# Kernel optimization log

Measured on AMD Instinct MI355X. Metric: run time of the kernel, lower is better.

Reference implementation:

```python
import jax, jax.numpy as jnp
import numpy as np

BN_EPS = 1e-5

def setup_inputs() -> dict:
    key = jax.random.key(0)
    ks = jax.random.split(key, 7)
    B, C_IN, C_P, N = 4, 256, 128, 4096
    sc_in = 1.0 / np.sqrt(C_IN)
    sc_p = 1.0 / np.sqrt(C_P)
    return {
        "x": jax.random.normal(ks[0], (B, C_IN, N), dtype=jnp.float32),
        "Wt": jax.random.normal(ks[1], (C_P, C_IN), dtype=jnp.float32) * sc_in,
        "Wp": jax.random.normal(ks[2], (C_P, C_IN), dtype=jnp.float32) * sc_in,
        "Wg": jax.random.normal(ks[3], (C_P, C_IN), dtype=jnp.float32) * sc_in,
        "Wz": jax.random.normal(ks[4], (C_IN, C_P), dtype=jnp.float32) * sc_p,
        "gamma": jnp.ones((C_IN,), dtype=jnp.float32),
        "beta": jnp.zeros((C_IN,), dtype=jnp.float32),
    }

def reference(x, Wt, Wp, Wg, Wz, gamma, beta):
    # x: [B, C_in, N]; 1x1 Conv1d == channel matmul
    t = jnp.einsum('oc,bcn->bon', Wt, x)   # [B, Cp, N]
    p = jnp.einsum('oc,bcn->bon', Wp, x)   # [B, Cp, N]
    g = jnp.einsum('oc,bcn->bon', Wg, x)   # [B, Cp, N]
    # att = bmm(t^T, p): [B, N, N]; softmax over dim=1 (non-standard axis)
    att = jnp.einsum('bcn,bcm->bnm', t, p)
    att = jax.nn.softmax(att, axis=1)
    # y = bmm(att, g^T): [B, N, Cp] -> permute to [B, Cp, N]
    y = jnp.einsum('bnm,bcm->bcn', att, g)
    z = jnp.einsum('oc,bcn->bon', Wz, y)   # [B, C_in, N]
    # BatchNorm1d (training-mode batch stats over batch+spatial)
    mean = jnp.mean(z, axis=(0, 2), keepdims=True)
    var = jnp.var(z, axis=(0, 2), keepdims=True)
    z_hat = (z - mean) * jax.lax.rsqrt(var + BN_EPS)
    out = z_hat * gamma[None, :, None] + beta[None, :, None] + x
    return out
```

## Files before the change

kernel.cpp:

```cpp
#include <hip/hip_runtime.h>
#include <hip/hip_fp16.h>

#define B_SZ 4
#define CIN  256
#define CP   128
#define NN   4096
#define NT   32
#define KSL  4

typedef _Float16 half_t;
typedef _Float16 f16x8 __attribute__((ext_vector_type(8)));
typedef float f32x4 __attribute__((ext_vector_type(4)));

#define GPTR(p) ((const __attribute__((address_space(1))) void*)(p))
#define LPTR(p) ((__attribute__((address_space(3))) void*)(p))

__device__ __forceinline__ float wave_sum64(float v){
  #pragma unroll
  for (int o = 32; o > 0; o >>= 1) v += __shfl_xor(v, o, 64);
  return v;
}

__global__ __launch_bounds__(256) void split_w(
    const float* __restrict__ Wt, const float* __restrict__ Wp,
    const float* __restrict__ Wg, half_t* __restrict__ Wh,
    half_t* __restrict__ Wl)
{
  const int sel = blockIdx.x;
  const float* W = (sel == 0) ? Wt : ((sel == 1) ? Wp : Wg);
  half_t* oh = Wh + sel * (CP * CIN);
  half_t* ol = Wl + sel * (CP * CIN);
  #pragma unroll
  for (int i = 0; i < 8; ++i){
    int i4 = blockIdx.y * 2048 + threadIdx.x + i * 256;
    float4 v = ((const float4*)W)[i4];
    v.x *= 16.f; v.y *= 16.f; v.z *= 16.f; v.w *= 16.f;
    union { half_t h[4]; uint2 u; } hh, ll;
    hh.h[0] = (half_t)v.x; ll.h[0] = (half_t)(v.x - (float)hh.h[0]);
    hh.h[1] = (half_t)v.y; ll.h[1] = (half_t)(v.y - (float)hh.h[1]);
    hh.h[2] = (half_t)v.z; ll.h[2] = (half_t)(v.z - (float)hh.h[2]);
    hh.h[3] = (half_t)v.w; ll.h[3] = (half_t)(v.w - (float)hh.h[3]);
    *(uint2*)(oh + i4 * 4) = hh.u;
    *(uint2*)(ol + i4 * 4) = ll.u;
  }
}

__global__ __launch_bounds__(256) void split_x(
    const float* __restrict__ x, half_t* __restrict__ xTh,
    half_t* __restrict__ xTl)
{
  const int b  = blockIdx.z;
  const int c0 = blockIdx.y * 64;
  const int n0 = blockIdx.x * 64;
  __shared__ float lds[64][68];
  const int tid = threadIdx.x;
  #pragma unroll
  for (int i = 0; i < 4; ++i){
    int idx = tid + i * 256;
    int cr = idx >> 4, nq = idx & 15;
    float4 v = *(const float4*)(x + ((size_t)b * CIN + c0 + cr) * NN + n0 + nq * 4);
    *(float4*)&lds[cr][nq * 4] = v;
  }
  __syncthreads();
  #pragma unroll
  for (int i = 0; i < 8; ++i){
    int idx = tid + i * 256;
    int nl = idx >> 5;
    int cp = (idx & 31) * 2;
    float v0 = lds[cp][nl], v1 = lds[cp + 1][nl];
    half_t h0 = (half_t)v0, h1 = (half_t)v1;
    half_t l0 = (half_t)(v0 - (float)h0), l1 = (half_t)(v1 - (float)h1);
    union { half_t h[2]; unsigned int u; } ph, pl;
    ph.h[0] = h0; ph.h[1] = h1;
    pl.h[0] = l0; pl.h[1] = l1;
    size_t o = ((size_t)b * NN + n0 + nl) * CIN + c0 + cp;
    *(unsigned int*)(xTh + o) = ph.u;
    *(unsigned int*)(xTl + o) = pl.u;
  }
}

__global__ __launch_bounds__(256) void tpg_gemm(
    const half_t* __restrict__ Wh, const half_t* __restrict__ Wl,
    const half_t* __restrict__ xTh, const half_t* __restrict__ xTl,
    half_t* __restrict__ tTh, half_t* __restrict__ tTl,
    half_t* __restrict__ pTh, half_t* __restrict__ pTl,
    half_t* __restrict__ gF)
{
  const int b   = blockIdx.z;
  const int sel = blockIdx.y;
  const int n0  = blockIdx.x * 64;
  const half_t* Ah_g = Wh + sel * (CP * CIN);
  const half_t* Al_g = Wl + sel * (CP * CIN);
  const half_t* Bh_g = xTh + ((size_t)b * NN + n0) * CIN;
  const half_t* Bl_g = xTl + ((size_t)b * NN + n0) * CIN;

  __shared__ half_t lds[24576];
  const int tid = threadIdx.x;
  const int wid = tid >> 6, lane = tid & 63;
  const int wo = wid >> 1, wn = wid & 1;
  const int lr = lane & 15, lq = lane >> 4;

  f32x4 acc[4][2];
  #pragma unroll
  for (int i = 0; i < 4; ++i)
    #pragma unroll
    for (int j = 0; j < 2; ++j) acc[i][j] = (f32x4){0.f,0.f,0.f,0.f};

  #pragma unroll 1
  for (int kc = 0; kc < CIN; kc += 64){
    #pragma unroll
    for (int it = 0; it < 4; ++it){
      int seg = wid * 4 + it;
      int row = seg * 8 + (lane >> 3);
      int us  = (lane & 7) ^ (row & 7);
      size_t go = (size_t)row * CIN + kc + us * 8;
      __builtin_amdgcn_global_load_lds(GPTR(Ah_g + go), LPTR(lds + seg*512), 16, 0, 0);
      __builtin_amdgcn_global_load_lds(GPTR(Al_g + go), LPTR(lds + 8192 + seg*512), 16, 0, 0);
    }
    #pragma unroll
    for (int it = 0; it < 2; ++it){
      int seg = wid * 2 + it;
      int row = seg * 8 + (lane >> 3);
      int us  = (lane & 7) ^ (row & 7);
      size_t go = (size_t)row * CIN + kc + us * 8;
      __builtin_amdgcn_global_load_lds(GPTR(Bh_g + go), LPTR(lds + 16384 + seg*512), 16, 0, 0);
      __builtin_amdgcn_global_load_lds(GPTR(Bl_g + go), LPTR(lds + 20480 + seg*512), 16, 0, 0);
    }
    asm volatile("s_waitcnt vmcnt(0)" ::: "memory");
    __syncthreads();

    #pragma unroll
    for (int kk = 0; kk < 2; ++kk){
      f16x8 ah[4], al4[4], bh[2], bl[2];
      #pragma unroll
      for (int f = 0; f < 4; ++f){
        int rA = wo * 64 + f * 16 + lr;
        int cA = (kk*32 + lq*8) ^ ((rA & 7) * 8);
        ah[f]  = *(const f16x8*)(lds + rA * 64 + cA);
        al4[f] = *(const f16x8*)(lds + 8192 + rA * 64 + cA);
      }
      #pragma unroll
      for (int f = 0; f < 2; ++f){
        int rB = wn * 32 + f * 16 + lr;
        int cB = (kk*32 + lq*8) ^ ((rB & 7) * 8);
        bh[f] = *(const f16x8*)(lds + 16384 + rB * 64 + cB);
        bl[f] = *(const f16x8*)(lds + 20480 + rB * 64 + cB);
      }
      #pragma unroll
      for (int fo = 0; fo < 4; ++fo)
        #pragma unroll
        for (int fn = 0; fn < 2; ++fn){
          acc[fo][fn] = __builtin_amdgcn_mfma_f32_16x16x32_f16(ah[fo],  bh[fn], acc[fo][fn], 0,0,0);
          acc[fo][fn] = __builtin_amdgcn_mfma_f32_16x16x32_f16(al4[fo], bh[fn], acc[fo][fn], 0,0,0);
          acc[fo][fn] = __builtin_amdgcn_mfma_f32_16x16x32_f16(ah[fo],  bl[fn], acc[fo][fn], 0,0,0);
        }
    }
    __syncthreads();
  }

  if (sel < 2){
    half_t* Ohi = ((sel == 0) ? tTh : pTh) + (size_t)b * NN * CP;
    half_t* Olo = ((sel == 0) ? tTl : pTl) + (size_t)b * NN * CP;
    float (*ldsT)[132] = (float (*)[132])lds;
    #pragma unroll
    for (int fo = 0; fo < 4; ++fo)
      #pragma unroll
      for (int fn = 0; fn < 2; ++fn)
        #pragma unroll
        for (int r = 0; r < 4; ++r){
          int n = wn * 32 + fn * 16 + lr;
          int o = wo * 64 + fo * 16 + lq * 4 + r;
          ldsT[n][o] = acc[fo][fn][r] * 0.0625f;
        }
    __syncthreads();
    #pragma unroll
    for (int it = 0; it < 16; ++it){
      int idx = tid + it * 256;
      int nl = idx >> 6;
      int cp = (idx & 63) * 2;
      float v0 = ldsT[nl][cp], v1 = ldsT[nl][cp + 1];
      half_t h0 = (half_t)v0, h1 = (half_t)v1;
      union { half_t h[2]; unsigned int u; } ph;
      ph.h[0] = h0; ph.h[1] = h1;
      *(unsigned int*)(Ohi + (size_t)(n0 + nl) * CP + cp) = ph.u;
      if (sel == 0){
        half_t l0 = (half_t)(v0 - (float)h0), l1 = (half_t)(v1 - (float)h1);
        union { half_t h[2]; unsigned int u; } pl;
        pl.h[0] = l0; pl.h[1] = l1;
        *(unsigned int*)(Olo + (size_t)(n0 + nl) * CP + cp) = pl.u;
      }
    }
  } else {
    half_t* G = gF + (size_t)b * CP * NN;
    #pragma unroll
    for (int fo = 0; fo < 4; ++fo)
      #pragma unroll
      for (int r = 0; r < 4; ++r){
        int o = wo * 64 + fo * 16 + lq * 4 + r;
        #pragma unroll
        for (int fn = 0; fn < 2; ++fn){
          int n = n0 + wn * 32 + fn * 16 + lr;
          G[(size_t)o * NN + n] = (half_t)(acc[fo][fn][r] * 0.0625f);
        }
      }
  }
}

__global__ __launch_bounds__(256) void s_gemm(
    const half_t* __restrict__ tTh, const half_t* __restrict__ tTl,
    const half_t* __restrict__ pTh,
    half_t* __restrict__ ST, float* __restrict__ pmax,
    float* __restrict__ psum)
{
  const int b  = blockIdx.z;
  const int m0 = blockIdx.x * 128;
  const int n0 = blockIdx.y * 128;
  const size_t tb = (size_t)b * NN * CP;
  half_t* STb = ST + (size_t)b * NN * NN;
  __shared__ half_t lds[3 * 128 * 64];
  const int tid = threadIdx.x;
  const int wid = tid >> 6, lane = tid & 63;
  const int wn = wid >> 1, wm = wid & 1;
  const int lr = lane & 15, lq = lane >> 4;

  f32x4 acc[4][4];
  #pragma unroll
  for (int i = 0; i < 4; ++i)
    #pragma unroll
    for (int j = 0; j < 4; ++j) acc[i][j] = (f32x4){0.f,0.f,0.f,0.f};

  const half_t* baseA_h = tTh + tb + (size_t)n0 * CP;
  const half_t* baseA_l = tTl + tb + (size_t)n0 * CP;
  const half_t* baseB_h = pTh + tb + (size_t)m0 * CP;

  #pragma unroll 1
  for (int kc = 0; kc < CP; kc += 64){
    #pragma unroll
    for (int it = 0; it < 4; ++it){
      int seg = wid * 4 + it;
      int row = seg * 8 + (lane >> 3);
      int us  = (lane & 7) ^ (row & 7);
      size_t go = (size_t)row * CP + kc + us * 8;
      __builtin_amdgcn_global_load_lds(GPTR(baseA_h + go), LPTR(lds + seg*512), 16, 0, 0);
      __builtin_amdgcn_global_load_lds(GPTR(baseA_l + go), LPTR(lds + 8192 + seg*512), 16, 0, 0);
      __builtin_amdgcn_global_load_lds(GPTR(baseB_h + go), LPTR(lds + 16384 + seg*512), 16, 0, 0);
    }
    asm volatile("s_waitcnt vmcnt(0)" ::: "memory");
    __syncthreads();

    #pragma unroll
    for (int kk = 0; kk < 2; ++kk){
      f16x8 ah[4], al[4], bh[4];
      #pragma unroll
      for (int f = 0; f < 4; ++f){
        int rA = wn*64 + f*16 + lr;
        int cA = (kk*32 + lq*8) ^ ((rA & 7) * 8);
        ah[f] = *(const f16x8*)(lds + rA*64 + cA);
        al[f] = *(const f16x8*)(lds + 8192 + rA*64 + cA);
        int rB = wm*64 + f*16 + lr;
        int cB = (kk*32 + lq*8) ^ ((rB & 7) * 8);
        bh[f] = *(const f16x8*)(lds + 16384 + rB*64 + cB);
      }
      #pragma unroll
      for (int fn = 0; fn < 4; ++fn)
        #pragma unroll
        for (int fm = 0; fm < 4; ++fm){
          acc[fn][fm] = __builtin_amdgcn_mfma_f32_16x16x32_f16(ah[fn], bh[fm], acc[fn][fm], 0,0,0);
          acc[fn][fm] = __builtin_amdgcn_mfma_f32_16x16x32_f16(al[fn], bh[fm], acc[fn][fm], 0,0,0);
        }
    }
    __syncthreads();
  }

  float* red  = (float*)lds;
  float* red2 = (float*)lds + 256;

  float cmax[4];
  #pragma unroll
  for (int fm = 0; fm < 4; ++fm){
    float t = -3.0e38f;
    #pragma unroll
    for (int fn = 0; fn < 4; ++fn)
      #pragma unroll
      for (int r = 0; r < 4; ++r) t = fmaxf(t, acc[fn][fm][r]);
    t = fmaxf(t, __shfl_xor(t, 16, 64));
    t = fmaxf(t, __shfl_xor(t, 32, 64));
    cmax[fm] = t;
  }
  if (lq == 0){
    #pragma unroll
    for (int fm = 0; fm < 4; ++fm) red[(wid*4+fm)*16 + lr] = cmax[fm];
  }
  __syncthreads();
  #pragma unroll
  for (int fm = 0; fm < 4; ++fm)
    cmax[fm] = fmaxf(red[((wm)*4+fm)*16 + lr], red[((2+wm)*4+fm)*16 + lr]);

  float csum[4] = {0.f, 0.f, 0.f, 0.f};
  #pragma unroll
  for (int fn = 0; fn < 4; ++fn)
    #pragma unroll
    for (int r = 0; r < 4; ++r){
      int n = n0 + wn*64 + fn*16 + lq*4 + r;
      half_t* dst = STb + (size_t)n * NN + m0 + wm*64;
      #pragma unroll
      for (int fm = 0; fm < 4; ++fm){
        float e = __expf(acc[fn][fm][r] - cmax[fm]);
        csum[fm] += e;
        dst[fm*16 + lr] = (half_t)e;
      }
    }
  #pragma unroll
  for (int fm = 0; fm < 4; ++fm){
    csum[fm] += __shfl_xor(csum[fm], 16, 64);
    csum[fm] += __shfl_xor(csum[fm], 32, 64);
  }
  __syncthreads();
  if (lq == 0){
    #pragma unroll
    for (int fm = 0; fm < 4; ++fm) red2[(wid*4+fm)*16 + lr] = csum[fm];
  }
  __syncthreads();
  if (wn == 0 && lq == 0){
    #pragma unroll
    for (int fm = 0; fm < 4; ++fm){
      int m = m0 + wm*64 + fm*16 + lr;
      pmax[((size_t)b * NT + blockIdx.y) * NN + m] = cmax[fm];
      psum[((size_t)b * NT + blockIdx.y) * NN + m] = red2[((wm)*4+fm)*16 + lr]
                                                   + red2[((2+wm)*4+fm)*16 + lr];
    }
  }
}

__global__ __launch_bounds__(256) void merge_corr(
    const float* __restrict__ pmax, const float* __restrict__ psum,
    float* __restrict__ corr)
{
  const size_t base = (size_t)blockIdx.y * NT * NN;
  const int m = blockIdx.x * 256 + threadIdx.x;
  float pm[NT];
  float mx = -3.0e38f;
  #pragma unroll
  for (int nt = 0; nt < NT; ++nt){
    pm[nt] = pmax[base + (size_t)nt * NN + m];
    mx = fmaxf(mx, pm[nt]);
  }
  float den = 0.f;
  #pragma unroll
  for (int nt = 0; nt < NT; ++nt){
    pm[nt] = __expf(pm[nt] - mx);
    den += psum[base + (size_t)nt * NN + m] * pm[nt];
  }
  const float r = 1.f / den;
  #pragma unroll
  for (int nt = 0; nt < NT; ++nt)
    corr[base + (size_t)nt * NN + m] = pm[nt] * r;
}

__global__ __launch_bounds__(256) void y_gemm(
    const half_t* __restrict__ gF, const half_t* __restrict__ ST,
    const float* __restrict__ corr, float* __restrict__ yp)
{
  const int b  = blockIdx.z;
  const int n0 = blockIdx.x * 64;
  const int nt = blockIdx.x >> 1;
  const int ks = blockIdx.y;
  const half_t* G   = gF + (size_t)b * CP * NN;
  const half_t* STb = ST + (size_t)b * NN * NN;
  const float* corb = corr + ((size_t)b * NT + nt) * NN;
  __shared__ half_t As[128*64];
  __shared__ half_t Bs[64*64];
  const int tid = threadIdx.x;
  const int wid = tid >> 6, lane = tid & 63;
  const int wc = wid >> 1, wn = wid & 1;
  const int lr = lane & 15, lq = lane >> 4;

  f32x4 acc[4][2];
  #pragma unroll
  for (int i = 0; i < 4; ++i)
    #pragma unroll
    for (int j = 0; j < 2; ++j) acc[i][j] = (f32x4){0.f,0.f,0.f,0.f};

  #pragma unroll 1
  for (int st = 0; st < 16; ++st){
    const int mc = ks * (NN / KSL) + st * 64;
    #pragma unroll
    for (int it = 0; it < 4; ++it){
      int seg = wid * 4 + it;
      int row = seg * 8 + (lane >> 3);
      int us  = (lane & 7) ^ (row & 7);
      __builtin_amdgcn_global_load_lds(GPTR(G + (size_t)row * NN + mc + us*8),
                                       LPTR(As + seg*512), 16, 0, 0);
    }
    #pragma unroll
    for (int i = 0; i < 4; ++i){
      int idx = tid + i * 256;
      int r = idx >> 4;
      int q = idx & 15;
      int mm = mc + q * 4;
      union { half_t h[4]; uint2 u2; } ev, eo;
      ev.u2 = *(const uint2*)(STb + (size_t)(n0 + r) * NN + mm);
      float4 cr = *(const float4*)(corb + mm);
      eo.h[0] = (half_t)((float)ev.h[0] * cr.x);
      eo.h[1] = (half_t)((float)ev.h[1] * cr.y);
      eo.h[2] = (half_t)((float)ev.h[2] * cr.z);
      eo.h[3] = (half_t)((float)ev.h[3] * cr.w);
      int c4 = (q * 4) ^ ((r & 7) * 8);
      *(uint2*)(Bs + r * 64 + c4) = eo.u2;
    }
    asm volatile("s_waitcnt vmcnt(0)" ::: "memory");
    __syncthreads();

    #pragma unroll
    for (int kk = 0; kk < 2; ++kk){
      f16x8 af[4], bf[2];
      #pragma unroll
      for (int f = 0; f < 4; ++f){
        int rA = wc*64 + f*16 + lr;
        af[f] = *(const f16x8*)(As + rA*64 + ((kk*32 + lq*8) ^ ((rA & 7)*8)));
      }
      #pragma unroll
      for (int f = 0; f < 2; ++f){
        int rB = wn*32 + f*16 + lr;
        bf[f] = *(const f16x8*)(Bs + rB*64 + ((kk*32 + lq*8) ^ ((rB & 7)*8)));
      }
      #pragma unroll
      for (int fc = 0; fc < 4; ++fc)
        #pragma unroll
        for (int fn = 0; fn < 2; ++fn)
          acc[fc][fn] = __builtin_amdgcn_mfma_f32_16x16x32_f16(af[fc], bf[fn], acc[fc][fn], 0,0,0);
    }
    __syncthreads();
  }
  #pragma unroll
  for (int fc = 0; fc < 4; ++fc)
    #pragma unroll
    for (int r = 0; r < 4; ++r){
      int c = wc*64 + fc*16 + lq*4 + r;
      float* dst = yp + (((size_t)b * KSL + ks) * CP + c) * NN + n0;
      #pragma unroll
      for (int fn = 0; fn < 2; ++fn) dst[wn*32 + fn*16 + lr] = acc[fc][fn][r];
    }
}

__global__ __launch_bounds__(256) void z_gemm(
    const float* __restrict__ Wz, const float* __restrict__ yp,
    float* __restrict__ z)
{
  const int b  = blockIdx.z;
  const int o0 = blockIdx.y * 128;
  const int n0 = blockIdx.x * 64;
  const float* y0 = yp + ((size_t)b * KSL + 0) * CP * NN;
  const float* y1 = yp + ((size_t)b * KSL + 1) * CP * NN;
  const float* y2 = yp + ((size_t)b * KSL + 2) * CP * NN;
  const float* y3 = yp + ((size_t)b * KSL + 3) * CP * NN;
  float* zb = z + (size_t)b * CIN * NN;

  __shared__ float a_s[32][132];
  __shared__ float b_s[32][64];

  const int tid = threadIdx.x;
  const int tx = tid & 15, ty = tid >> 4;

  float acc[2][4][4];
  #pragma unroll
  for (int qa = 0; qa < 2; ++qa)
    #pragma unroll
    for (int i = 0; i < 4; ++i)
      #pragma unroll
      for (int j = 0; j < 4; ++j) acc[qa][i][j] = 0.f;

  for (int k0 = 0; k0 < CP; k0 += 32){
    #pragma unroll
    for (int i = 0; i < 4; ++i){
      int f4i = tid + i * 256;
      int c  = f4i >> 3;
      int k4 = f4i & 7;
      float4 w = *(const float4*)(Wz + (size_t)(o0 + c) * CP + k0 + k4 * 4);
      a_s[k4*4+0][c] = w.x;
      a_s[k4*4+1][c] = w.y;
      a_s[k4*4+2][c] = w.z;
      a_s[k4*4+3][c] = w.w;
    }
    #pragma unroll
    for (int i = 0; i < 2; ++i){
      int f4i = tid + i * 256;
      int kk = f4i >> 4;
      int n4 = f4i & 15;
      const size_t off = (size_t)(k0 + kk) * NN + n0 + n4 * 4;
      float4 v0 = *(const float4*)(y0 + off);
      float4 v1 = *(const float4*)(y1 + off);
      float4 v2 = *(const float4*)(y2 + off);
      float4 v3 = *(const float4*)(y3 + off);
      float4 sv;
      sv.x = v0.x + v1.x + v2.x + v3.x;
      sv.y = v0.y + v1.y + v2.y + v3.y;
      sv.z = v0.z + v1.z + v2.z + v3.z;
      sv.w = v0.w + v1.w + v2.w + v3.w;
      *(float4*)&b_s[kk][n4*4] = sv;
    }
    __syncthreads();
    #pragma unroll
    for (int kk = 0; kk < 32; ++kk){
      float af[8], bf[4];
      *(float4*)&af[0] = *(const float4*)&a_s[kk][ty*4];
      *(float4*)&af[4] = *(const float4*)&a_s[kk][ty*4+64];
      *(float4*)&bf[0] = *(const float4*)&b_s[kk][tx*4];
      #pragma unroll
      for (int qa = 0; qa < 2; ++qa)
        #pragma unroll
        for (int i = 0; i < 4; ++i)
          #pragma unroll
          for (int j = 0; j < 4; ++j)
            acc[qa][i][j] = fmaf(af[qa*4+i], bf[j], acc[qa][i][j]);
    }
    __syncthreads();
  }
  #pragma unroll
  for (int qa = 0; qa < 2; ++qa)
    #pragma unroll
    for (int i = 0; i < 4; ++i){
      const int row = o0 + qa*64 + ty*4 + i;
      float4 v = make_float4(acc[qa][i][0], acc[qa][i][1],
                             acc[qa][i][2], acc[qa][i][3]);
      *(float4*)(zb + (size_t)row * NN + n0 + tx*4) = v;
    }
}

__global__ __launch_bounds__(256) void bn_stats(
    const float* __restrict__ z, float* __restrict__ mean,
    float* __restrict__ rstd)
{
  const int c = blockIdx.x;
  const int tid = threadIdx.x;
  float s = 0.f, s2 = 0.f;
  for (int b = 0; b < B_SZ; ++b){
    const float4* row = (const float4*)(z + ((size_t)b * CIN + c) * NN);
    #pragma unroll
    for (int i = 0; i < 4; ++i){
      float4 v = row[tid + i*256];
      s  += v.x + v.y + v.z + v.w;
      s2 += v.x*v.x + v.y*v.y + v.z*v.z + v.w*v.w;
    }
  }
  s  = wave_sum64(s);
  s2 = wave_sum64(s2);
  __shared__ float rs[4];
  __shared__ float rq[4];
  const int wid = tid >> 6, lane = tid & 63;
  if (lane == 0){ rs[wid] = s; rq[wid] = s2; }
  __syncthreads();
  if (tid == 0){
    const float S1 = rs[0]+rs[1]+rs[2]+rs[3];
    const float S2 = rq[0]+rq[1]+rq[2]+rq[3];
    const float inv = 1.f / (float)(B_SZ * NN);
    const float m = S1 * inv;
    const float var = S2 * inv - m * m;
    mean[c] = m;
    rstd[c] = 1.f / sqrtf(var + 1e-5f);
  }
}

__global__ __launch_bounds__(256) void finalize_k(
    const float* __restrict__ z, const float* __restrict__ x,
    const float* __restrict__ mean, const float* __restrict__ rstd,
    const float* __restrict__ gamma, const float* __restrict__ beta,
    float* __restrict__ out)
{
  const int total = B_SZ * CIN * NN / 4;
  for (int i = blockIdx.x * blockDim.x + threadIdx.x; i < total;
       i += gridDim.x * blockDim.x){
    const int c = (i >> 10) & (CIN - 1);
    float4 zv = ((const float4*)z)[i];
    float4 xv = ((const float4*)x)[i];
    const float m = mean[c], r = rstd[c], ga = gamma[c], be = beta[c];
    float4 o;
    o.x = (zv.x - m) * r * ga + be + xv.x;
    o.y = (zv.y - m) * r * ga + be + xv.y;
    o.z = (zv.z - m) * r * ga + be + xv.z;
    o.w = (zv.w - m) * r * ga + be + xv.w;
    ((float4*)out)[i] = o;
  }
}

extern "C" void kernel_launch(void* const* d_in, const int* in_sizes, int n_in,
                              void* d_out, int out_size, void* d_ws, size_t ws_size,
                              hipStream_t stream)
{
  const float* x     = (const float*)d_in[0];
  const float* Wt    = (const float*)d_in[1];
  const float* Wp    = (const float*)d_in[2];
  const float* Wg    = (const float*)d_in[3];
  const float* Wz    = (const float*)d_in[4];
  const float* gamma = (const float*)d_in[5];
  const float* beta  = (const float*)d_in[6];
  float* out = (float*)d_out;

  float* wsf = (float*)d_ws;
  size_t off = 0;
  half_t* ST  = (half_t*)(wsf + off); off += (size_t)B_SZ * NN * NN / 2;
  half_t* tTh = (half_t*)(wsf + off); off += (size_t)B_SZ*NN*CP/2;
  half_t* tTl = (half_t*)(wsf + off); off += (size_t)B_SZ*NN*CP/2;
  half_t* pTh = (half_t*)(wsf + off); off += (size_t)B_SZ*NN*CP/2;
  half_t* pTl = (half_t*)(wsf + off); off += (size_t)B_SZ*NN*CP/2;
  half_t* gF  = (half_t*)(wsf + off); off += (size_t)B_SZ*CP*NN/2;
  half_t* xTh = (half_t*)(wsf + off); off += (size_t)B_SZ*NN*CIN/2;
  half_t* xTl = (half_t*)(wsf + off); off += (size_t)B_SZ*NN*CIN/2;
  half_t* Wh  = (half_t*)(wsf + off); off += (size_t)3*CP*CIN/2;
  half_t* Wl  = (half_t*)(wsf + off); off += (size_t)3*CP*CIN/2;
  float*  yp  = wsf + off; off += (size_t)B_SZ * KSL * CP * NN;
  float*  pmax= wsf + off; off += (size_t)B_SZ * NT * NN;
  float*  psum= wsf + off; off += (size_t)B_SZ * NT * NN;
  float*  corr= wsf + off; off += (size_t)B_SZ * NT * NN;
  float*  meanb = wsf + off; off += CIN;
  float*  rstdb = wsf + off; off += CIN;
  float*  z = (float*)ST;

  split_w <<<dim3(3, 4),           256, 0, stream>>>(Wt, Wp, Wg, Wh, Wl);
  split_x <<<dim3(64, 4, B_SZ),    256, 0, stream>>>(x, xTh, xTl);
  tpg_gemm<<<dim3(64, 3, B_SZ),    256, 0, stream>>>(Wh, Wl, xTh, xTl,
                                                     tTh, tTl, pTh, pTl, gF);
  s_gemm    <<<dim3(32, 32, B_SZ), 256, 0, stream>>>(tTh, tTl, pTh,
                                                     ST, pmax, psum);
  merge_corr<<<dim3(16, B_SZ),     256, 0, stream>>>(pmax, psum, corr);
  y_gemm    <<<dim3(64, KSL, B_SZ),256, 0, stream>>>(gF, ST, corr, yp);
  z_gemm    <<<dim3(64, 2, B_SZ),  256, 0, stream>>>(Wz, yp, z);
  bn_stats  <<<dim3(CIN),          256, 0, stream>>>(z, meanb, rstdb);
  finalize_k<<<dim3(2048),         256, 0, stream>>>(z, x, meanb, rstdb,
                                                     gamma, beta, out);
}
```

Before: 230.0 us.

## Drop low-half split for t in S GEMM and widen y_gemm N tile

Removes the fp16 hi/lo split of t so the attention-score GEMM uses a single fp16 product instead of two MFMAs per fragment, which halves its MFMA work and cuts its LDS and global traffic by a third. Separately, y_gemm tiles are widened from 64 to 128 columns, halving the grid and reusing each loaded g tile across more outputs. The precision reduction risks larger error in the attention logits before softmax.

```diff
diff --git a/kernel.cpp b/kernel.cpp
--- a/kernel.cpp
+++ b/kernel.cpp
@@ -82,8 +82,7 @@
 __global__ __launch_bounds__(256) void tpg_gemm(
     const half_t* __restrict__ Wh, const half_t* __restrict__ Wl,
     const half_t* __restrict__ xTh, const half_t* __restrict__ xTl,
-    half_t* __restrict__ tTh, half_t* __restrict__ tTl,
-    half_t* __restrict__ pTh, half_t* __restrict__ pTl,
+    half_t* __restrict__ tT, half_t* __restrict__ pT,
     half_t* __restrict__ gF)
 {
   const int b   = blockIdx.z;
@@ -159,8 +158,7 @@
   }
 
   if (sel < 2){
-    half_t* Ohi = ((sel == 0) ? tTh : pTh) + (size_t)b * NN * CP;
-    half_t* Olo = ((sel == 0) ? tTl : pTl) + (size_t)b * NN * CP;
+    half_t* Ohi = ((sel == 0) ? tT : pT) + (size_t)b * NN * CP;
     float (*ldsT)[132] = (float (*)[132])lds;
     #pragma unroll
     for (int fo = 0; fo < 4; ++fo)
@@ -179,16 +177,9 @@
       int nl = idx >> 6;
       int cp = (idx & 63) * 2;
       float v0 = ldsT[nl][cp], v1 = ldsT[nl][cp + 1];
-      half_t h0 = (half_t)v0, h1 = (half_t)v1;
       union { half_t h[2]; unsigned int u; } ph;
-      ph.h[0] = h0; ph.h[1] = h1;
+      ph.h[0] = (half_t)v0; ph.h[1] = (half_t)v1;
       *(unsigned int*)(Ohi + (size_t)(n0 + nl) * CP + cp) = ph.u;
-      if (sel == 0){
-        half_t l0 = (half_t)(v0 - (float)h0), l1 = (half_t)(v1 - (float)h1);
-        union { half_t h[2]; unsigned int u; } pl;
-        pl.h[0] = l0; pl.h[1] = l1;
-        *(unsigned int*)(Olo + (size_t)(n0 + nl) * CP + cp) = pl.u;
-      }
     }
   } else {
     half_t* G = gF + (size_t)b * CP * NN;
@@ -207,8 +198,7 @@
 }
 
 __global__ __launch_bounds__(256) void s_gemm(
-    const half_t* __restrict__ tTh, const half_t* __restrict__ tTl,
-    const half_t* __restrict__ pTh,
+    const half_t* __restrict__ tT, const half_t* __restrict__ pT,
     half_t* __restrict__ ST, float* __restrict__ pmax,
     float* __restrict__ psum)
 {
@@ -217,7 +207,7 @@
   const int n0 = blockIdx.y * 128;
   const size_t tb = (size_t)b * NN * CP;
   half_t* STb = ST + (size_t)b * NN * NN;
-  __shared__ half_t lds[3 * 128 * 64];
+  __shared__ half_t lds[2 * 128 * 64];
   const int tid = threadIdx.x;
   const int wid = tid >> 6, lane = tid & 63;
   const int wn = wid >> 1, wm = wid & 1;
@@ -229,9 +219,8 @@
     #pragma unroll
     for (int j = 0; j < 4; ++j) acc[i][j] = (f32x4){0.f,0.f,0.f,0.f};
 
-  const half_t* baseA_h = tTh + tb + (size_t)n0 * CP;
-  const half_t* baseA_l = tTl + tb + (size_t)n0 * CP;
-  const half_t* baseB_h = pTh + tb + (size_t)m0 * CP;
+  const half_t* baseA = tT + tb + (size_t)n0 * CP;
+  const half_t* baseB = pT + tb + (size_t)m0 * CP;
 
   #pragma unroll 1
   for (int kc = 0; kc < CP; kc += 64){
@@ -241,33 +230,27 @@
       int row = seg * 8 + (lane >> 3);
       int us  = (lane & 7) ^ (row & 7);
       size_t go = (size_t)row * CP + kc + us * 8;
-      __builtin_amdgcn_global_load_lds(GPTR(baseA_h + go), LPTR(lds + seg*512), 16, 0, 0);
-      __builtin_amdgcn_global_load_lds(GPTR(baseA_l + go), LPTR(lds + 8192 + seg*512), 16, 0, 0);
-      __builtin_amdgcn_global_load_lds(GPTR(baseB_h + go), LPTR(lds + 16384 + seg*512), 16, 0, 0);
+      __builtin_amdgcn_global_load_lds(GPTR(baseA + go), LPTR(lds + seg*512), 16, 0, 0);
+      __builtin_amdgcn_global_load_lds(GPTR(baseB + go), LPTR(lds + 8192 + seg*512), 16, 0, 0);
     }
     asm volatile("s_waitcnt vmcnt(0)" ::: "memory");
     __syncthreads();
 
     #pragma unroll
     for (int kk = 0; kk < 2; ++kk){
-      f16x8 ah[4], al[4], bh[4];
+      f16x8 ah[4], bh[4];
       #pragma unroll
       for (int f = 0; f < 4; ++f){
         int rA = wn*64 + f*16 + lr;
-        int cA = (kk*32 + lq*8) ^ ((rA & 7) * 8);
-        ah[f] = *(const f16x8*)(lds + rA*64 + cA);
-        al[f] = *(const f16x8*)(lds + 8192 + rA*64 + cA);
+        ah[f] = *(const f16x8*)(lds + rA*64 + ((kk*32 + lq*8) ^ ((rA & 7) * 8)));
         int rB = wm*64 + f*16 + lr;
-        int cB = (kk*32 + lq*8) ^ ((rB & 7) * 8);
-        bh[f] = *(const f16x8*)(lds + 16384 + rB*64 + cB);
+        bh[f] = *(const f16x8*)(lds + 8192 + rB*64 + ((kk*32 + lq*8) ^ ((rB & 7) * 8)));
       }
       #pragma unroll
       for (int fn = 0; fn < 4; ++fn)
         #pragma unroll
-        for (int fm = 0; fm < 4; ++fm){
+        for (int fm = 0; fm < 4; ++fm)
           acc[fn][fm] = __builtin_amdgcn_mfma_f32_16x16x32_f16(ah[fn], bh[fm], acc[fn][fm], 0,0,0);
-          acc[fn][fm] = __builtin_amdgcn_mfma_f32_16x16x32_f16(al[fn], bh[fm], acc[fn][fm], 0,0,0);
-        }
     }
     __syncthreads();
   }
@@ -362,24 +345,24 @@
     const float* __restrict__ corr, float* __restrict__ yp)
 {
   const int b  = blockIdx.z;
-  const int n0 = blockIdx.x * 64;
-  const int nt = blockIdx.x >> 1;
+  const int nt = blockIdx.x;
+  const int n0 = nt * 128;
   const int ks = blockIdx.y;
   const half_t* G   = gF + (size_t)b * CP * NN;
   const half_t* STb = ST + (size_t)b * NN * NN;
   const float* corb = corr + ((size_t)b * NT + nt) * NN;
   __shared__ half_t As[128*64];
-  __shared__ half_t Bs[64*64];
+  __shared__ half_t Bs[128*64];
   const int tid = threadIdx.x;
   const int wid = tid >> 6, lane = tid & 63;
   const int wc = wid >> 1, wn = wid & 1;
   const int lr = lane & 15, lq = lane >> 4;
 
-  f32x4 acc[4][2];
+  f32x4 acc[4][4];
   #pragma unroll
   for (int i = 0; i < 4; ++i)
     #pragma unroll
-    for (int j = 0; j < 2; ++j) acc[i][j] = (f32x4){0.f,0.f,0.f,0.f};
+    for (int j = 0; j < 4; ++j) acc[i][j] = (f32x4){0.f,0.f,0.f,0.f};
 
   #pragma unroll 1
   for (int st = 0; st < 16; ++st){
@@ -393,7 +376,7 @@
                                        LPTR(As + seg*512), 16, 0, 0);
     }
     #pragma unroll
-    for (int i = 0; i < 4; ++i){
+    for (int i = 0; i < 8; ++i){
       int idx = tid + i * 256;
       int r = idx >> 4;
       int q = idx & 15;
@@ -413,21 +396,18 @@
 
     #pragma unroll
     for (int kk = 0; kk < 2; ++kk){
-      f16x8 af[4], bf[2];
+      f16x8 af[4], bf[4];
       #pragma unroll
       for (int f = 0; f < 4; ++f){
         int rA = wc*64 + f*16 + lr;
         af[f] = *(const f16x8*)(As + rA*64 + ((kk*32 + lq*8) ^ ((rA & 7)*8)));
-      }
-      #pragma unroll
-      for (int f = 0; f < 2; ++f){
-        int rB = wn*32 + f*16 + lr;
+        int rB = wn*64 + f*16 + lr;
         bf[f] = *(const f16x8*)(Bs + rB*64 + ((kk*32 + lq*8) ^ ((rB & 7)*8)));
       }
       #pragma unroll
       for (int fc = 0; fc < 4; ++fc)
         #pragma unroll
-        for (int fn = 0; fn < 2; ++fn)
+        for (int fn = 0; fn < 4; ++fn)
           acc[fc][fn] = __builtin_amdgcn_mfma_f32_16x16x32_f16(af[fc], bf[fn], acc[fc][fn], 0,0,0);
     }
     __syncthreads();
@@ -439,7 +419,7 @@
       int c = wc*64 + fc*16 + lq*4 + r;
       float* dst = yp + (((size_t)b * KSL + ks) * CP + c) * NN + n0;
       #pragma unroll
-      for (int fn = 0; fn < 2; ++fn) dst[wn*32 + fn*16 + lr] = acc[fc][fn][r];
+      for (int fn = 0; fn < 4; ++fn) dst[wn*64 + fn*16 + lr] = acc[fc][fn][r];
     }
 }
 
@@ -599,10 +579,8 @@
   float* wsf = (float*)d_ws;
   size_t off = 0;
   half_t* ST  = (half_t*)(wsf + off); off += (size_t)B_SZ * NN * NN / 2;
-  half_t* tTh = (half_t*)(wsf + off); off += (size_t)B_SZ*NN*CP/2;
-  half_t* tTl = (half_t*)(wsf + off); off += (size_t)B_SZ*NN*CP/2;
-  half_t* pTh = (half_t*)(wsf + off); off += (size_t)B_SZ*NN*CP/2;
-  half_t* pTl = (half_t*)(wsf + off); off += (size_t)B_SZ*NN*CP/2;
+  half_t* tT  = (half_t*)(wsf + off); off += (size_t)B_SZ*NN*CP/2;
+  half_t* pT  = (half_t*)(wsf + off); off += (size_t)B_SZ*NN*CP/2;
   half_t* gF  = (half_t*)(wsf + off); off += (size_t)B_SZ*CP*NN/2;
   half_t* xTh = (half_t*)(wsf + off); off += (size_t)B_SZ*NN*CIN/2;
   half_t* xTl = (half_t*)(wsf + off); off += (size_t)B_SZ*NN*CIN/2;
@@ -619,11 +597,10 @@
   split_w <<<dim3(3, 4),           256, 0, stream>>>(Wt, Wp, Wg, Wh, Wl);
   split_x <<<dim3(64, 4, B_SZ),    256, 0, stream>>>(x, xTh, xTl);
   tpg_gemm<<<dim3(64, 3, B_SZ),    256, 0, stream>>>(Wh, Wl, xTh, xTl,
-                                                     tTh, tTl, pTh, pTl, gF);
-  s_gemm    <<<dim3(32, 32, B_SZ), 256, 0, stream>>>(tTh, tTl, pTh,
-                                                     ST, pmax, psum);
+                                                     tT, pT, gF);
+  s_gemm    <<<dim3(32, 32, B_SZ), 256, 0, stream>>>(tT, pT, ST, pmax, psum);
   merge_corr<<<dim3(16, B_SZ),     256, 0, stream>>>(pmax, psum, corr);
-  y_gemm    <<<dim3(64, KSL, B_SZ),256, 0, stream>>>(gF, ST, corr, yp);
+  y_gemm    <<<dim3(32, KSL, B_SZ),256, 0, stream>>>(gF, ST, corr, yp);
   z_gemm    <<<dim3(64, 2, B_SZ),  256, 0, stream>>>(Wz, yp, z);
   bn_stats  <<<dim3(CIN),          256, 0, stream>>>(z, meanb, rstdb);
   finalize_k<<<dim3(2048),         256, 0, stream>>>(z, x, meanb, rstdb,
```

Result: faster. 220.8 us (-4.0%).
